# Kernel optimization log

Measured on AMD Instinct MI355X. Metric: run time of the kernel, lower is better.

Reference implementation:

```python
import jax, jax.numpy as jnp
import numpy as np

B, C, N = 4, 32, 256
D_IN, D_EMB, K = 512, 1024, 4096  # input_dim, llm_embedding_dim, codebook_size
EPS = 1e-12


def setup_inputs() -> dict:
    key = jax.random.key(0)
    ks = jax.random.split(key, 6)
    s_in = float(1.0 / np.sqrt(D_IN))
    s_emb = float(1.0 / np.sqrt(D_EMB))
    return {
        "x": jax.random.normal(ks[0], (B, C, N, D_IN), jnp.float32),
        # nn.Linear(input_dim, llm_embedding_dim): weight [out, in], uniform(-1/sqrt(in), 1/sqrt(in))
        "w_in": jax.random.uniform(ks[1], (D_EMB, D_IN), jnp.float32, -s_in, s_in),
        "b_in": jax.random.uniform(ks[2], (D_EMB,), jnp.float32, -s_in, s_in),
        "w_out": jax.random.uniform(ks[3], (D_IN, D_EMB), jnp.float32, -s_emb, s_emb),
        "b_out": jax.random.uniform(ks[4], (D_IN,), jnp.float32, -s_emb, s_emb),
        # frozen LLM-embedding codebook (copied from llm_embedding_bank, requires_grad=False)
        "codebook": jax.random.normal(ks[5], (K, D_EMB), jnp.float32),
    }


def _rotate_to(src, tgt):
    # Rotation trick (arXiv:2410.06424, sec 4.2) as in vector-quantize-pytorch.
    # Forward value equals tgt; gradient flows through src via a (detached)
    # Householder rotation + scaling.
    n_src = jnp.linalg.norm(src, axis=-1, keepdims=True)
    n_tgt = jnp.linalg.norm(tgt, axis=-1, keepdims=True)
    u = jax.lax.stop_gradient(src / jnp.maximum(n_src, EPS))   # unit src, detached
    q = tgt / jnp.maximum(n_tgt, EPS)                          # unit tgt (codebook: no grad)
    w = u + q
    w = jax.lax.stop_gradient(w / jnp.maximum(jnp.linalg.norm(w, axis=-1, keepdims=True), EPS))
    rot = (src
           - 2.0 * jnp.sum(src * w, -1, keepdims=True) * w
           + 2.0 * jnp.sum(src * u, -1, keepdims=True) * q)
    return rot * jax.lax.stop_gradient(n_tgt / jnp.maximum(n_src, EPS))


def reference(x, w_in, b_in, w_out, b_out, codebook):
    Bb, Cc, Nn, _ = x.shape
    # input projection, flatten channels x patches into token axis
    z = jnp.einsum('bcnd,ed->bcne', x, w_in) + b_in          # [B, C, N, D_EMB]
    z = z.reshape(Bb, Cc * Nn, -1)                           # [B, T, D_EMB]
    # squared euclidean distances to codebook: ||z||^2 - 2 z.c + ||c||^2
    dists = (jnp.sum(z * z, -1, keepdims=True)
             - 2.0 * jnp.einsum('bte,ke->btk', z, codebook)
             + jnp.sum(codebook * codebook, -1))             # [B, T, K]
    indices = jnp.argmin(dists, axis=-1)                     # [B, T] int
    q = codebook[indices]                                    # gather [B, T, D_EMB]
    quantized = _rotate_to(z, q)                             # == q in value
    # commitment loss (commitment_weight = 1.0); codebook frozen -> only commit term
    aux_loss = jnp.mean((jax.lax.stop_gradient(quantized) - z) ** 2)
    out = jnp.einsum('bte,de->btd', quantized, w_out) + b_out
    return (out.reshape(Bb, Cc, Nn, -1),
            indices,
            quantized.reshape(Bb, Cc, Nn, -1),
            aux_loss)
```

## Files before the change

kernel.cpp:

```cpp
#include <hip/hip_runtime.h>

#define M_TOK 32768
#define DIN   512
#define DEMB  1024
#define KC    4096

#define IDX_OFF ((size_t)M_TOK * DIN)
#define Q_OFF   (IDX_OFF + M_TOK)
#define AUX_OFF (Q_OFF + (size_t)M_TOK * DEMB)

typedef _Float16 f16x8 __attribute__((ext_vector_type(8)));
typedef _Float16 f16x4 __attribute__((ext_vector_type(4)));
typedef float f32x4 __attribute__((ext_vector_type(4)));

__device__ inline void gload16(const void* g, void* s) {
    __builtin_amdgcn_global_load_lds((const __attribute__((address_space(1))) void*)g,
                                     (__attribute__((address_space(3))) void*)s, 16, 0, 0);
}

__device__ inline unsigned umin2(unsigned a, unsigned b) { return a < b ? a : b; }
__device__ inline unsigned umax2(unsigned a, unsigned b) { return a > b ? a : b; }

__device__ inline float block_reduce_sum_256(float v) {
#pragma unroll
    for (int off = 32; off > 0; off >>= 1) v += __shfl_down(v, off);
    __shared__ float smem[4];
    const int lane = threadIdx.x & 63;
    const int w = threadIdx.x >> 6;
    if (lane == 0) smem[w] = v;
    __syncthreads();
    return smem[0] + smem[1] + smem[2] + smem[3];
}

__global__ __launch_bounds__(256) void prep_all(const float* __restrict__ cb,
                                                const float* __restrict__ w_out,
                                                const float* __restrict__ w_in,
                                                _Float16* __restrict__ cbf,
                                                _Float16* __restrict__ wok,
                                                _Float16* __restrict__ wpk,
                                                _Float16* __restrict__ cbp,
                                                float* __restrict__ cn2p,
                                                float* __restrict__ aux) {
    const int b = blockIdx.x;
    if (b < 4096) {
        if (b == 0 && threadIdx.x == 0) *aux = 0.0f;
        const float4 v = reinterpret_cast<const float4*>(cb + (size_t)b * DEMB)[threadIdx.x];
        f16x4 h;
        h[0] = (_Float16)v.x; h[1] = (_Float16)v.y; h[2] = (_Float16)v.z; h[3] = (_Float16)v.w;
        reinterpret_cast<f16x4*>(cbf + (size_t)b * DEMB)[threadIdx.x] = h;
        float s = v.x * v.x + v.y * v.y + v.z * v.z + v.w * v.w;
        s = block_reduce_sum_256(s);
        if (threadIdx.x == 0) cn2p[b] = 0.5f * s + 1024.0f;
    } else if (b < 4352) {
        const int id = (b - 4096) * 256 + threadIdx.x;
        const int l = id & 63;
        const int c16 = (id >> 6) & 31;
        const int kk = id >> 11;
        const int col = c16 * 16 + (l & 15);
        const int kb = kk * 32 + (l >> 4) * 8;
        const float* src = w_out + (size_t)col * DEMB + kb;
        const float4 a = *reinterpret_cast<const float4*>(src);
        const float4 b4 = *reinterpret_cast<const float4*>(src + 4);
        f16x8 h;
        h[0] = (_Float16)a.x; h[1] = (_Float16)a.y; h[2] = (_Float16)a.z; h[3] = (_Float16)a.w;
        h[4] = (_Float16)b4.x; h[5] = (_Float16)b4.y; h[6] = (_Float16)b4.z; h[7] = (_Float16)b4.w;
        *reinterpret_cast<f16x8*>(wok + (size_t)id * 8) = h;
    } else if (b < 6400) {
        const int id = (b - 4352) * 256 + threadIdx.x;
        const int c16 = id >> 11;
        const int rem = id & 2047;
        const int kk = rem >> 6;
        const int l = rem & 63;
        const int lgq = l >> 4, lcq = l & 15;
        const float* src = cb + ((size_t)(c16 * 16 + lcq)) * DEMB + kk * 32 + lgq * 8;
        const float4 a = *reinterpret_cast<const float4*>(src);
        const float4 b4 = *reinterpret_cast<const float4*>(src + 4);
        f16x8 h;
        h[0] = (_Float16)a.x; h[1] = (_Float16)a.y; h[2] = (_Float16)a.z; h[3] = (_Float16)a.w;
        h[4] = (_Float16)b4.x; h[5] = (_Float16)b4.y; h[6] = (_Float16)b4.z; h[7] = (_Float16)b4.w;
        const int ntile = c16 >> 2, nn = c16 & 3;
        const size_t off = ((size_t)(kk * 256 + ntile * 4 + nn)) * 64 + l;
        *reinterpret_cast<f16x8*>(cbp + off * 8) = h;
    } else {
        const int id = (b - 6400) * 256 + threadIdx.x;
        const int l = id & 63;
        const int hl = (id >> 6) & 1;
        const int c16 = (id >> 7) & 63;
        const int kk = id >> 13;
        const int col = c16 * 16 + (l & 15);
        const int kb = kk * 32 + (l >> 4) * 8;
        const float* src = w_in + (size_t)col * DIN + kb;
        const float4 a = *reinterpret_cast<const float4*>(src);
        const float4 b4 = *reinterpret_cast<const float4*>(src + 4);
        const float e[8] = {a.x, a.y, a.z, a.w, b4.x, b4.y, b4.z, b4.w};
        f16x8 o;
#pragma unroll
        for (int j = 0; j < 8; ++j) {
            const _Float16 hv = (_Float16)e[j];
            o[j] = hl ? (_Float16)((e[j] - (float)hv) * 2048.0f) : hv;
        }
        *reinterpret_cast<f16x8*>(wpk + (size_t)id * 8) = o;
    }
}

__global__ void __launch_bounds__(512)
__attribute__((amdgpu_waves_per_eu(2, 2)))
zgemm_stream(const float* __restrict__ x,
             const _Float16* __restrict__ wpk,
             const float* __restrict__ bin,
             float* __restrict__ zq,
             _Float16* __restrict__ zf) {
    extern __shared__ _Float16 sm[];
    _Float16* Ah = sm;
    _Float16* Al = sm + 32768;
    const int t = threadIdx.x;
    const int w = t >> 6, l = t & 63;
    const int lg = l >> 4, lc = l & 15;
    const int m0 = blockIdx.x * 64;

    {
        const int r = t >> 3;
        const int c0 = t & 7;
#pragma unroll
        for (int i = 0; i < 8; ++i) {
            const int c = c0 + i * 8;
            const float* px = x + (size_t)(m0 + r) * DIN + c * 8;
            const float4 a = *reinterpret_cast<const float4*>(px);
            const float4 b4 = *reinterpret_cast<const float4*>(px + 4);
            const float e[8] = {a.x, a.y, a.z, a.w, b4.x, b4.y, b4.z, b4.w};
            f16x8 h, lo;
#pragma unroll
            for (int j = 0; j < 8; ++j) {
                const _Float16 hv = (_Float16)e[j];
                h[j] = hv;
                lo[j] = (_Float16)((e[j] - (float)hv) * 2048.0f);
            }
            const int swz = (c & 0x30) | ((c ^ r) & 15);
            *reinterpret_cast<f16x8*>(Ah + (size_t)(r * 64 + swz) * 8) = h;
            *reinterpret_cast<f16x8*>(Al + (size_t)(r * 64 + swz) * 8) = lo;
        }
    }

    const char* ztb = (const char*)sm;
    int lbase[4][4];
#pragma unroll
    for (int m = 0; m < 4; ++m)
#pragma unroll
        for (int j = 0; j < 4; ++j)
            lbase[m][j] = (m * 16 + lc) * 1024 + ((((j * 4) | lg) ^ lc) & 15) * 16;

    const char* pL = (const char*)wpk + w * 4096 + l * 16;

    f16x8 bh[2][2], bl[2][2];
#pragma unroll
    for (int s = 0; s < 2; ++s)
#pragma unroll
        for (int n = 0; n < 2; ++n) {
            bh[s][n] = *reinterpret_cast<const f16x8*>(pL + s * 131072 + n * 2048);
            bl[s][n] = *reinterpret_cast<const f16x8*>(pL + s * 131072 + n * 2048 + 1024);
        }

    __syncthreads();

    f16x8 ah[2][4], al[2][4];
#pragma unroll
    for (int m = 0; m < 4; ++m) {
        ah[0][m] = *reinterpret_cast<const f16x8*>(ztb + lbase[m][0]);
        al[0][m] = *reinterpret_cast<const f16x8*>(ztb + 65536 + lbase[m][0]);
    }

    unsigned boff = 2u * 131072u;
    for (int p = 0; p < 4; ++p) {
        f32x4 acc1[4][2], acc2[4][2];
#pragma unroll
        for (int n = 0; n < 2; ++n) {
            const float bb = bin[p * 256 + w * 32 + n * 16 + lc];
#pragma unroll
            for (int m = 0; m < 4; ++m) {
                acc1[m][n] = (f32x4){bb, bb, bb, bb};
                acc2[m][n] = (f32x4){0.f, 0.f, 0.f, 0.f};
            }
        }
        const unsigned wrapAdd = (unsigned)((p < 3 ? 1 : -3) * 32768 - 15 * 131072);
#pragma unroll
        for (int kk = 0; kk < 16; ++kk) {
            const int nk = (kk + 1) & 15;
#pragma unroll
            for (int m = 0; m < 4; ++m) {
                ah[(kk + 1) & 1][m] = *reinterpret_cast<const f16x8*>(
                    ztb + lbase[m][nk & 3] + ((nk >> 2) << 8));
                al[(kk + 1) & 1][m] = *reinterpret_cast<const f16x8*>(
                    ztb + 65536 + lbase[m][nk & 3] + ((nk >> 2) << 8));
            }
            __builtin_amdgcn_s_setprio(1);
#pragma unroll
            for (int m = 0; m < 4; ++m)
#pragma unroll
                for (int n = 0; n < 2; ++n) {
                    acc1[m][n] = __builtin_amdgcn_mfma_f32_16x16x32_f16(
                        ah[kk & 1][m], bh[kk & 1][n], acc1[m][n], 0, 0, 0);
                    acc2[m][n] = __builtin_amdgcn_mfma_f32_16x16x32_f16(
                        ah[kk & 1][m], bl[kk & 1][n], acc2[m][n], 0, 0, 0);
                    acc2[m][n] = __builtin_amdgcn_mfma_f32_16x16x32_f16(
                        al[kk & 1][m], bh[kk & 1][n], acc2[m][n], 0, 0, 0);
                }
            __builtin_amdgcn_s_setprio(0);
#pragma unroll
            for (int n = 0; n < 2; ++n) {
                bh[kk & 1][n] = *reinterpret_cast<const f16x8*>(pL + boff + n * 2048);
                bl[kk & 1][n] = *reinterpret_cast<const f16x8*>(pL + boff + n * 2048 + 1024);
            }
            boff += (kk == 13) ? wrapAdd : 131072u;
        }
#pragma unroll
        for (int n = 0; n < 2; ++n) {
            const int col = p * 256 + w * 32 + n * 16 + lc;
#pragma unroll
            for (int m = 0; m < 4; ++m)
#pragma unroll
                for (int rg = 0; rg < 4; ++rg) {
                    const int row = m0 + m * 16 + lg * 4 + rg;
                    const float z = acc1[m][n][rg] + acc2[m][n][rg] * (1.0f / 2048.0f);
                    zq[(size_t)row * DEMB + col] = z;
                    zf[(size_t)row * DEMB + col] = (_Float16)(-z);
                }
        }
    }
}

__global__ void __launch_bounds__(512)
__attribute__((amdgpu_waves_per_eu(2, 2)))
dist_topk(const _Float16* __restrict__ zf,
          const _Float16* __restrict__ cbp,
          const float* __restrict__ cn2p,
          unsigned* __restrict__ pk) {
    extern __shared__ _Float16 zt[];
    const int t = threadIdx.x;
    const int w = t >> 6, l = t & 63;
    const int lg = l >> 4, lc = l & 15;
    const int m0 = blockIdx.x * 64;

    {
        const int r0 = t >> 7;
        const int ch = t & 127;
#pragma unroll
        for (int i = 0; i < 16; ++i) {
            const int row = i * 4 + r0;
            const int sch = (ch & 0x70) | ((ch ^ row) & 15);
            gload16(zf + (((size_t)(m0 + row)) << 10) + sch * 8,
                    zt + ((size_t)(i * 512 + t)) * 8);
        }
    }

    const char* ztb = (const char*)zt;
    int lbase[4][4];
#pragma unroll
    for (int m = 0; m < 4; ++m)
#pragma unroll
        for (int j = 0; j < 4; ++j)
            lbase[m][j] = (m * 16 + lc) * 2048 + ((((j * 4) | lg) ^ lc) << 4);

    unsigned k0[16], k1[16];
#pragma unroll
    for (int r = 0; r < 16; ++r) { k0[r] = 0xFFFFFFFFu; k1[r] = 0xFFFFFFFFu; }

    const char* pL = (const char*)cbp + l * 16;

    f16x8 bf[4][4];
    {
#pragma unroll
        for (int s = 0; s < 4; ++s)
#pragma unroll
            for (int n = 0; n < 4; ++n)
                bf[s][n] = *reinterpret_cast<const f16x8*>(pL + s * 262144 + w * 4096 + n * 1024);
    }
    __syncthreads();

    f16x8 af[4][4];
#pragma unroll
    for (int s = 0; s < 2; ++s)
#pragma unroll
        for (int m = 0; m < 4; ++m)
            af[s][m] = *reinterpret_cast<const f16x8*>(ztb + lbase[m][s] + ((s & 28) << 6));

    unsigned boff = (unsigned)(w * 4096 + 4 * 262144);
    for (int nt8 = 0; nt8 < 8; ++nt8) {
        const int ntile = nt8 * 8 + w;
        const unsigned wrapAdd = (unsigned)((nt8 < 7 ? 8 : -56) * 4096 - 31 * 262144);
        const int colb = ntile * 64;
        unsigned colw[4];
        float c2[4];
#pragma unroll
        for (int n = 0; n < 4; ++n) {
            colw[n] = (unsigned)(colb + n * 16 + lc);
            c2[n] = cn2p[colw[n]];
        }
        f32x4 acc[4][4];
#pragma unroll
        for (int m = 0; m < 4; ++m)
#pragma unroll
            for (int n = 0; n < 4; ++n)
                acc[m][n] = (f32x4){c2[n], c2[n], c2[n], c2[n]};

#pragma unroll
        for (int kk = 0; kk < 32; ++kk) {
            const int nk2 = (kk + 2) & 31;
#pragma unroll
            for (int m = 0; m < 4; ++m)
                af[(kk + 2) & 3][m] = *reinterpret_cast<const f16x8*>(
                    ztb + lbase[m][nk2 & 3] + ((nk2 & 28) << 6));
            __builtin_amdgcn_s_setprio(1);
#pragma unroll
            for (int m = 0; m < 4; ++m)
#pragma unroll
                for (int n = 0; n < 4; ++n)
                    acc[m][n] = __builtin_amdgcn_mfma_f32_16x16x32_f16(
                        af[kk & 3][m], bf[kk & 3][n], acc[m][n], 0, 0, 0);
            __builtin_amdgcn_s_setprio(0);
#pragma unroll
            for (int n = 0; n < 4; ++n)
                bf[kk & 3][n] = *reinterpret_cast<const f16x8*>(pL + boff + n * 1024);
            boff += (kk == 27) ? wrapAdd : 262144u;
        }

#pragma unroll
        for (int n = 0; n < 4; ++n) {
#pragma unroll
            for (int m = 0; m < 4; ++m)
#pragma unroll
                for (int rg = 0; rg < 4; ++rg) {
                    const unsigned key =
                        (__float_as_uint(acc[m][n][rg]) & 0xFFFFF000u) | colw[n];
                    const int r = m * 4 + rg;
                    const unsigned kmax = umax2(k0[r], key);
                    k0[r] = umin2(k0[r], key);
                    k1[r] = umin2(k1[r], kmax);
                }
        }
    }
#pragma unroll
    for (int off = 1; off < 16; off <<= 1) {
#pragma unroll
        for (int r = 0; r < 16; ++r) {
            const unsigned b0 = __shfl_xor(k0[r], off);
            const unsigned b1 = __shfl_xor(k1[r], off);
            const unsigned lo = umin2(k0[r], b0);
            const unsigned hi = umax2(k0[r], b0);
            k0[r] = lo;
            k1[r] = umin2(hi, umin2(k1[r], b1));
        }
    }
    if (lc == 0) {
#pragma unroll
        for (int m = 0; m < 4; ++m)
#pragma unroll
            for (int rg = 0; rg < 4; ++rg) {
                const int r = m * 4 + rg;
                const int tok = m0 + m * 16 + lg * 4 + rg;
                pk[(size_t)(w * 2 + 0) * M_TOK + tok] = k0[r];
                pk[(size_t)(w * 2 + 1) * M_TOK + tok] = k1[r];
            }
    }
}

__global__ __launch_bounds__(256) void refine_idx(const float* __restrict__ cb,
                                                  const float* __restrict__ cn2p,
                                                  const unsigned* __restrict__ pk,
                                                  float* __restrict__ zq,
                                                  float* __restrict__ idx_f,
                                                  int* __restrict__ idx_i,
                                                  float* __restrict__ aux) {
    const int wv = threadIdx.x >> 6;
    const int t = blockIdx.x * 4 + wv;
    const int l = threadIdx.x & 63;
    float4* zp = reinterpret_cast<float4*>(zq + ((size_t)t << 10));
    float4 zr[4];
#pragma unroll
    for (int j = 0; j < 4; ++j) zr[j] = zp[l + j * 64];

    float zn = 0.0f;
#pragma unroll
    for (int j = 0; j < 4; ++j) {
        zn = fmaf(zr[j].x, zr[j].x, zn);
        zn = fmaf(zr[j].y, zr[j].y, zn);
        zn = fmaf(zr[j].z, zr[j].z, zn);
        zn = fmaf(zr[j].w, zr[j].w, zn);
    }
#pragma unroll
    for (int off = 1; off < 64; off <<= 1) zn += __shfl_xor(zn, off);

    unsigned v = 0xFFFFFFFFu;
    if (l < 16) v = pk[(size_t)l * M_TOK + t];

    float bestd = 3.4e38f;
    int besti = 0x7fffffff;
#pragma unroll
    for (int s = 0; s < 4; ++s) {
        unsigned mv = v;
#pragma unroll
        for (int off = 1; off < 64; off <<= 1) mv = umin2(mv, __shfl_xor(mv, off));
        if (v == mv) v = 0xFFFFFFFFu;
        const int mi = (int)(mv & 0xFFFu);
        const float4* cp = reinterpret_cast<const float4*>(cb + ((size_t)mi << 10));
        float s4 = 0.0f;
#pragma unroll
        for (int j = 0; j < 4; ++j) {
            const float4 c = cp[l + j * 64];
            s4 = fmaf(zr[j].x, c.x, s4);
            s4 = fmaf(zr[j].y, c.y, s4);
            s4 = fmaf(zr[j].z, c.z, s4);
            s4 = fmaf(zr[j].w, c.w, s4);
        }
#pragma unroll
        for (int off = 1; off < 64; off <<= 1) s4 += __shfl_xor(s4, off);
        const float d = cn2p[mi] - s4;
        if (d < bestd || (d == bestd && mi < besti)) { bestd = d; besti = mi; }
    }
    const float4* cpb = reinterpret_cast<const float4*>(cb + ((size_t)besti << 10));
#pragma unroll
    for (int j = 0; j < 4; ++j) zp[l + j * 64] = cpb[l + j * 64];

    __shared__ float dsum[4];
    if (l == 0) {
        idx_f[t] = (float)besti;
        idx_i[t] = besti;
        dsum[wv] = 2.0f * bestd - 2048.0f + zn;
    }
    __syncthreads();
    if (threadIdx.x == 0)
        atomicAdd(aux, (dsum[0] + dsum[1] + dsum[2] + dsum[3]) * (1.0f / 33554432.0f));
}

__global__ void __launch_bounds__(512)
__attribute__((amdgpu_waves_per_eu(2, 2)))
outgemm_stream(const _Float16* __restrict__ cbf,
               const _Float16* __restrict__ wok,
               const float* __restrict__ bout,
               const int* __restrict__ idx,
               float* __restrict__ out) {
    extern __shared__ _Float16 at[];
    const int t = threadIdx.x;
    const int w = t >> 6, l = t & 63;
    const int lg = l >> 4, lc = l & 15;
    const int m0 = blockIdx.x * 64;

    {
        const int r0 = t >> 7;
        const int ch = t & 127;
#pragma unroll
        for (int i = 0; i < 16; ++i) {
            const int row = i * 4 + r0;
            const int gi = idx[m0 + row];
            const int sch = (ch & 0x70) | ((ch ^ row) & 15);
            gload16(cbf + (((size_t)gi) << 10) + sch * 8,
                    at + ((size_t)(i * 512 + t)) * 8);
        }
    }

    const char* ztb = (const char*)at;
    int lbase[4][4];
#pragma unroll
    for (int m = 0; m < 4; ++m)
#pragma unroll
        for (int j = 0; j < 4; ++j)
            lbase[m][j] = (m * 16 + lc) * 2048 + ((((j * 4) | lg) ^ lc) << 4);

    const char* pL = (const char*)wok + l * 16;

    f16x8 bf[4][4];
    {
#pragma unroll
        for (int s = 0; s < 4; ++s)
#pragma unroll
            for (int n = 0; n < 4; ++n)
                bf[s][n] = *reinterpret_cast<const f16x8*>(pL + s * 32768 + w * 4096 + n * 1024);
    }
    __syncthreads();

    f16x8 af[4][4];
#pragma unroll
    for (int s = 0; s < 2; ++s)
#pragma unroll
        for (int m = 0; m < 4; ++m)
            af[s][m] = *reinterpret_cast<const f16x8*>(ztb + lbase[m][s] + ((s & 28) << 6));

    f32x4 acc[4][4];
#pragma unroll
    for (int n = 0; n < 4; ++n) {
        const float bb = bout[w * 64 + n * 16 + lc];
#pragma unroll
        for (int m = 0; m < 4; ++m)
            acc[m][n] = (f32x4){bb, bb, bb, bb};
    }

    unsigned boff = (unsigned)(w * 4096 + 4 * 32768);
#pragma unroll
    for (int kk = 0; kk < 32; ++kk) {
        const int nk2 = (kk + 2) & 31;
#pragma unroll
        for (int m = 0; m < 4; ++m)
            af[(kk + 2) & 3][m] = *reinterpret_cast<const f16x8*>(
                ztb + lbase[m][nk2 & 3] + ((nk2 & 28) << 6));
        __builtin_amdgcn_s_setprio(1);
#pragma unroll
        for (int m = 0; m < 4; ++m)
#pragma unroll
            for (int n = 0; n < 4; ++n)
                acc[m][n] = __builtin_amdgcn_mfma_f32_16x16x32_f16(
                    af[kk & 3][m], bf[kk & 3][n], acc[m][n], 0, 0, 0);
        __builtin_amdgcn_s_setprio(0);
#pragma unroll
        for (int n = 0; n < 4; ++n)
            bf[kk & 3][n] = *reinterpret_cast<const f16x8*>(pL + boff + n * 1024);
        boff += (kk == 27) ? (unsigned)(-(28 * 32768)) : 32768u;
    }

#pragma unroll
    for (int n = 0; n < 4; ++n) {
        const int col = w * 64 + n * 16 + lc;
#pragma unroll
        for (int m = 0; m < 4; ++m)
#pragma unroll
            for (int rg = 0; rg < 4; ++rg) {
                const int row = m0 + m * 16 + lg * 4 + rg;
                out[(size_t)row * DIN + col] = acc[m][n][rg];
            }
    }
}

extern "C" void kernel_launch(void* const* d_in, const int* in_sizes, int n_in,
                              void* d_out, int out_size, void* d_ws, size_t ws_size,
                              hipStream_t stream) {
    const float* x = (const float*)d_in[0];
    const float* w_in = (const float*)d_in[1];
    const float* b_in = (const float*)d_in[2];
    const float* w_out = (const float*)d_in[3];
    const float* b_out = (const float*)d_in[4];
    const float* cb = (const float*)d_in[5];

    float* out = (float*)d_out;
    float* idx_f = out + IDX_OFF;
    float* zq = out + Q_OFF;
    float* aux = out + AUX_OFF;
    _Float16* zf = (_Float16*)d_out;

    char* ws = (char*)d_ws;
    float* cn2p = (float*)ws;
    int* idx_i = (int*)(ws + 16384);
    unsigned* pk = (unsigned*)(ws + 147456);
    _Float16* cbf = (_Float16*)(ws + 4341760);
    _Float16* cbp = (_Float16*)(ws + 12730368);
    _Float16* wpk = (_Float16*)(ws + 21118976);
    _Float16* wok = (_Float16*)(ws + 23216128);

    prep_all<<<6912, 256, 0, stream>>>(cb, w_out, w_in, cbf, wok, wpk, cbp, cn2p, aux);
    zgemm_stream<<<M_TOK / 64, 512, 131072, stream>>>(x, wpk, b_in, zq, zf);
    dist_topk<<<M_TOK / 64, 512, 131072, stream>>>(zf, cbp, cn2p, pk);
    refine_idx<<<M_TOK / 4, 256, 0, stream>>>(cb, cn2p, pk, zq, idx_f, idx_i, aux);
    outgemm_stream<<<M_TOK / 64, 512, 131072, stream>>>(cbf, wok, b_out, idx_i, out);
}
```

Before: 520.3 us.

## Fuse top-k distance search and fp32 refinement into one kernel via LDS

The fp16 distance/top-k kernel and the separate fp32 refinement kernel are merged. Candidate keys now go through shared memory instead of a global pk buffer, and each wave then refines 8 of the block's 64 tokens. This removes one launch, the global round trip of the candidate list, and most aux atomics, since there is now one atomic per wave instead of per 4-token block. In exchange, the latency-bound refinement phase runs inside a kernel limited to 2 waves per EU with large LDS, so it may hide memory latency less well than the separate high-occupancy launch.

```diff
diff --git a/kernel.cpp b/kernel.cpp
--- a/kernel.cpp
+++ b/kernel.cpp
@@ -230,10 +230,14 @@
 
 __global__ void __launch_bounds__(512)
 __attribute__((amdgpu_waves_per_eu(2, 2)))
-dist_topk(const _Float16* __restrict__ zf,
-          const _Float16* __restrict__ cbp,
-          const float* __restrict__ cn2p,
-          unsigned* __restrict__ pk) {
+dist_refine(const _Float16* __restrict__ zf,
+            const _Float16* __restrict__ cbp,
+            const float* __restrict__ cn2p,
+            const float* __restrict__ cb,
+            float* __restrict__ zq,
+            float* __restrict__ idx_f,
+            int* __restrict__ idx_i,
+            float* __restrict__ aux) {
     extern __shared__ _Float16 zt[];
     const int t = threadIdx.x;
     const int w = t >> 6, l = t & 63;
@@ -350,85 +354,80 @@
             k1[r] = umin2(hi, umin2(k1[r], b1));
         }
     }
+
+    __syncthreads();
+    unsigned* pks = (unsigned*)zt;
     if (lc == 0) {
 #pragma unroll
         for (int m = 0; m < 4; ++m)
 #pragma unroll
             for (int rg = 0; rg < 4; ++rg) {
                 const int r = m * 4 + rg;
-                const int tok = m0 + m * 16 + lg * 4 + rg;
-                pk[(size_t)(w * 2 + 0) * M_TOK + tok] = k0[r];
-                pk[(size_t)(w * 2 + 1) * M_TOK + tok] = k1[r];
-            }
-    }
-}
-
-__global__ __launch_bounds__(256) void refine_idx(const float* __restrict__ cb,
-                                                  const float* __restrict__ cn2p,
-                                                  const unsigned* __restrict__ pk,
-                                                  float* __restrict__ zq,
-                                                  float* __restrict__ idx_f,
-                                                  int* __restrict__ idx_i,
-                                                  float* __restrict__ aux) {
-    const int wv = threadIdx.x >> 6;
-    const int t = blockIdx.x * 4 + wv;
-    const int l = threadIdx.x & 63;
-    float4* zp = reinterpret_cast<float4*>(zq + ((size_t)t << 10));
-    float4 zr[4];
-#pragma unroll
-    for (int j = 0; j < 4; ++j) zr[j] = zp[l + j * 64];
-
-    float zn = 0.0f;
-#pragma unroll
-    for (int j = 0; j < 4; ++j) {
-        zn = fmaf(zr[j].x, zr[j].x, zn);
-        zn = fmaf(zr[j].y, zr[j].y, zn);
-        zn = fmaf(zr[j].z, zr[j].z, zn);
-        zn = fmaf(zr[j].w, zr[j].w, zn);
-    }
-#pragma unroll
-    for (int off = 1; off < 64; off <<= 1) zn += __shfl_xor(zn, off);
-
-    unsigned v = 0xFFFFFFFFu;
-    if (l < 16) v = pk[(size_t)l * M_TOK + t];
-
-    float bestd = 3.4e38f;
-    int besti = 0x7fffffff;
-#pragma unroll
-    for (int s = 0; s < 4; ++s) {
-        unsigned mv = v;
-#pragma unroll
-        for (int off = 1; off < 64; off <<= 1) mv = umin2(mv, __shfl_xor(mv, off));
-        if (v == mv) v = 0xFFFFFFFFu;
-        const int mi = (int)(mv & 0xFFFu);
-        const float4* cp = reinterpret_cast<const float4*>(cb + ((size_t)mi << 10));
-        float s4 = 0.0f;
+                const int tloc = m * 16 + lg * 4 + rg;
+                pks[(w * 2 + 0) * 64 + tloc] = k0[r];
+                pks[(w * 2 + 1) * 64 + tloc] = k1[r];
+            }
+    }
+    __syncthreads();
+
+    float asum = 0.0f;
+    for (int i = 0; i < 8; ++i) {
+        const int tloc = w * 8 + i;
+        const int tok = m0 + tloc;
+        float4* zp = reinterpret_cast<float4*>(zq + ((size_t)tok << 10));
+        float4 zr[4];
+#pragma unroll
+        for (int j = 0; j < 4; ++j) zr[j] = zp[l + j * 64];
+
+        float zn = 0.0f;
 #pragma unroll
         for (int j = 0; j < 4; ++j) {
-            const float4 c = cp[l + j * 64];
-            s4 = fmaf(zr[j].x, c.x, s4);
-            s4 = fmaf(zr[j].y, c.y, s4);
-            s4 = fmaf(zr[j].z, c.z, s4);
-            s4 = fmaf(zr[j].w, c.w, s4);
-        }
-#pragma unroll
-        for (int off = 1; off < 64; off <<= 1) s4 += __shfl_xor(s4, off);
-        const float d = cn2p[mi] - s4;
-        if (d < bestd || (d == bestd && mi < besti)) { bestd = d; besti = mi; }
-    }
-    const float4* cpb = reinterpret_cast<const float4*>(cb + ((size_t)besti << 10));
-#pragma unroll
-    for (int j = 0; j < 4; ++j) zp[l + j * 64] = cpb[l + j * 64];
-
-    __shared__ float dsum[4];
-    if (l == 0) {
-        idx_f[t] = (float)besti;
-        idx_i[t] = besti;
-        dsum[wv] = 2.0f * bestd - 2048.0f + zn;
-    }
-    __syncthreads();
-    if (threadIdx.x == 0)
-        atomicAdd(aux, (dsum[0] + dsum[1] + dsum[2] + dsum[3]) * (1.0f / 33554432.0f));
+            zn = fmaf(zr[j].x, zr[j].x, zn);
+            zn = fmaf(zr[j].y, zr[j].y, zn);
+            zn = fmaf(zr[j].z, zr[j].z, zn);
+            zn = fmaf(zr[j].w, zr[j].w, zn);
+        }
+#pragma unroll
+        for (int off = 1; off < 64; off <<= 1) zn += __shfl_xor(zn, off);
+
+        unsigned v = 0xFFFFFFFFu;
+        if (l < 16) v = pks[l * 64 + tloc];
+
+        float bestd = 3.4e38f;
+        int besti = 0x7fffffff;
+#pragma unroll
+        for (int s = 0; s < 4; ++s) {
+            unsigned mv = v;
+#pragma unroll
+            for (int off = 1; off < 64; off <<= 1) mv = umin2(mv, __shfl_xor(mv, off));
+            if (v == mv) v = 0xFFFFFFFFu;
+            const int mi = (int)(mv & 0xFFFu);
+            const float4* cp = reinterpret_cast<const float4*>(cb + ((size_t)mi << 10));
+            float s4 = 0.0f;
+#pragma unroll
+            for (int j = 0; j < 4; ++j) {
+                const float4 c = cp[l + j * 64];
+                s4 = fmaf(zr[j].x, c.x, s4);
+                s4 = fmaf(zr[j].y, c.y, s4);
+                s4 = fmaf(zr[j].z, c.z, s4);
+                s4 = fmaf(zr[j].w, c.w, s4);
+            }
+#pragma unroll
+            for (int off = 1; off < 64; off <<= 1) s4 += __shfl_xor(s4, off);
+            const float d = cn2p[mi] - s4;
+            if (d < bestd || (d == bestd && mi < besti)) { bestd = d; besti = mi; }
+        }
+        const float4* cpb = reinterpret_cast<const float4*>(cb + ((size_t)besti << 10));
+#pragma unroll
+        for (int j = 0; j < 4; ++j) zp[l + j * 64] = cpb[l + j * 64];
+
+        if (l == 0) {
+            idx_f[tok] = (float)besti;
+            idx_i[tok] = besti;
+            asum += 2.0f * bestd - 2048.0f + zn;
+        }
+    }
+    if (l == 0) atomicAdd(aux, asum * (1.0f / 33554432.0f));
 }
 
 __global__ void __launch_bounds__(512)
@@ -547,7 +546,6 @@
     char* ws = (char*)d_ws;
     float* cn2p = (float*)ws;
     int* idx_i = (int*)(ws + 16384);
-    unsigned* pk = (unsigned*)(ws + 147456);
     _Float16* cbf = (_Float16*)(ws + 4341760);
     _Float16* cbp = (_Float16*)(ws + 12730368);
     _Float16* wpk = (_Float16*)(ws + 21118976);
@@ -555,7 +553,6 @@
 
     prep_all<<<6912, 256, 0, stream>>>(cb, w_out, w_in, cbf, wok, wpk, cbp, cn2p, aux);
     zgemm_stream<<<M_TOK / 64, 512, 131072, stream>>>(x, wpk, b_in, zq, zf);
-    dist_topk<<<M_TOK / 64, 512, 131072, stream>>>(zf, cbp, cn2p, pk);
-    refine_idx<<<M_TOK / 4, 256, 0, stream>>>(cb, cn2p, pk, zq, idx_f, idx_i, aux);
+    dist_refine<<<M_TOK / 64, 512, 131072, stream>>>(zf, cbp, cn2p, cb, zq, idx_f, idx_i, aux);
     outgemm_stream<<<M_TOK / 64, 512, 131072, stream>>>(cbf, wok, b_out, idx_i, out);
 }
```

After: 493.8 us. 5.1% less time.
